# Kernel tuning notes

Measured on AMD Instinct MI355X. Metric: run time of the kernel, lower is better.

The kernel has to match this reference:

```python
import jax, jax.numpy as jnp
import numpy as np

DIM = 1024
T = 16384
WINDOW = 32
DIM_HEAD = 64
HEADS = DIM // DIM_HEAD  # 16
EPS = 1e-5


def setup_inputs() -> dict:
    key = jax.random.key(0)
    k1, k2, k3 = jax.random.split(key, 3)
    x = jax.random.normal(k1, (DIM, T), dtype=jnp.float32)
    w_qkv = jax.random.normal(k2, (3 * DIM, DIM), dtype=jnp.float32) / np.float32(np.sqrt(DIM))
    w_out = jax.random.normal(k3, (DIM, DIM), dtype=jnp.float32) / np.float32(np.sqrt(DIM))
    gamma = jnp.ones((DIM,), dtype=jnp.float32)
    beta = jnp.zeros((DIM,), dtype=jnp.float32)
    return {"x": x, "w_qkv": w_qkv, "w_out": w_out, "gamma": gamma, "beta": beta}


def _rotate_half(t):
    # original: split channels into (2, d/2), swap halves with negation
    d = t.shape[-1]
    return jnp.concatenate((-t[..., d // 2:], t[..., :d // 2]), axis=-1)


def reference(x, w_qkv, w_out, gamma, beta):
    C, Tn = x.shape
    xt = x.T  # (T, C)
    # LayerNorm over channel dim (eqx.nn.LayerNorm, eps=1e-5)
    mu = jnp.mean(xt, axis=-1, keepdims=True)
    var = jnp.var(xt, axis=-1, keepdims=True)
    normed = (xt - mu) * jax.lax.rsqrt(var + EPS) * gamma + beta
    # QKV projection (Linear with weight (out,in), no bias)
    qkv = normed @ w_qkv.T  # (T, 3C)
    q, k, v = jnp.split(qkv, 3, axis=-1)
    w = Tn // WINDOW
    def towin(t):  # (w n) (h d) -> h w n d
        return t.reshape(w, WINDOW, HEADS, DIM_HEAD).transpose(2, 0, 1, 3)
    q, k, v = map(towin, (q, k, v))
    # rotary pos emb over window positions (use_xpos=False -> scale == 1)
    inv_freq = 1.0 / (10000.0 ** (jnp.arange(0, DIM_HEAD, 2, dtype=jnp.float32) / DIM_HEAD))
    tpos = jnp.arange(WINDOW, dtype=jnp.float32)
    freqs = jnp.einsum('i,j->ij', tpos, inv_freq)  # (n, d/2)
    freqs = jnp.concatenate((freqs, freqs), axis=-1)  # (n, d)
    cos, sin = jnp.cos(freqs), jnp.sin(freqs)
    q = q * cos + _rotate_half(q) * sin
    k = k * cos + _rotate_half(k) * sin
    # per-head, per-window full (non-causal) attention
    scale = DIM_HEAD ** -0.5
    logits = jnp.einsum('hwnd,hwmd->hwnm', q, k) * scale
    attn = jax.nn.softmax(logits, axis=-1)
    out = jnp.einsum('hwnm,hwmd->hwnd', attn, v)
    out = out.transpose(1, 2, 0, 3).reshape(Tn, C)  # h w n d -> (w n) (h d)
    out = out @ w_out.T
    return out.T + x
```

## Files before the change

kernel.cpp:

```cpp
#include <hip/hip_runtime.h>

#define T_TOK 16384
#define C_DIM 1024

typedef float f32x4 __attribute__((ext_vector_type(4)));
typedef float f32x16 __attribute__((ext_vector_type(16)));
typedef __bf16 bf16x8 __attribute__((ext_vector_type(8)));
typedef unsigned short u16x8 __attribute__((ext_vector_type(8)));
typedef unsigned short u16x4 __attribute__((ext_vector_type(4)));

__device__ __forceinline__ unsigned short f2bf(float f) {
  union { float f; unsigned u; } v; v.f = f;
  unsigned r = v.u + 0x7fffu + ((v.u >> 16) & 1u);
  return (unsigned short)(r >> 16);
}
__device__ __forceinline__ float bf2f(unsigned short h) {
  union { unsigned u; float f; } v; v.u = ((unsigned)h) << 16;
  return v.f;
}
__device__ __forceinline__ unsigned pk2(float a, float b) {
  return (unsigned)f2bf(a) | ((unsigned)f2bf(b) << 16);
}

__global__ __launch_bounds__(256) void cvt_kernel(const float* __restrict__ in,
                                                  unsigned short* __restrict__ out, int n4) {
  int i = blockIdx.x * 256 + threadIdx.x;
  if (i >= n4) return;
  f32x4 v = *(const f32x4*)(in + (size_t)i * 4);
  u16x4 o;
#pragma unroll
  for (int j = 0; j < 4; ++j) o[j] = f2bf(v[j]);
  *(u16x4*)(out + (size_t)i * 4) = o;
}

__global__ __launch_bounds__(256) void rope_tab_kernel(float* __restrict__ tab) {
  int idx = blockIdx.x * 256 + threadIdx.x;
  if (idx >= 1024) return;
  int mm = idx >> 5, d = idx & 31;
  float invf = powf(10000.f, -(float)d * (1.f / 32.f));
  float ang = (float)mm * invf;
  float s, c;
  sincosf(ang, &s, &c);
  tab[idx * 2] = c;
  tab[idx * 2 + 1] = s;
}

__global__ __launch_bounds__(256) void ln_stats_kernel(const float* __restrict__ x,
                                                       float* __restrict__ mu,
                                                       float* __restrict__ rstd) {
  __shared__ float s1[4][64];
  __shared__ float s2[4][64];
  const int tid = threadIdx.x;
  const int lt = tid & 63, cq = tid >> 6;
  const int t = blockIdx.x * 64 + lt;
  float s = 0.f, ss = 0.f;
  const float* p = x + (size_t)cq * 256 * T_TOK + t;
  for (int c = 0; c < 256; ++c) {
    float v = p[(size_t)c * T_TOK];
    s += v; ss += v * v;
  }
  s1[cq][lt] = s; s2[cq][lt] = ss;
  __syncthreads();
  if (tid < 64) {
    float S  = s1[0][tid] + s1[1][tid] + s1[2][tid] + s1[3][tid];
    float SS = s2[0][tid] + s2[1][tid] + s2[2][tid] + s2[3][tid];
    float m = S * (1.f / 1024.f);
    float var = SS * (1.f / 1024.f) - m * m;
    mu[blockIdx.x * 64 + tid] = m;
    rstd[blockIdx.x * 64 + tid] = rsqrtf(var + 1e-5f);
  }
}

__global__ __launch_bounds__(256) void ln_tr_kernel(const float* __restrict__ x,
                                                    const float* __restrict__ mu,
                                                    const float* __restrict__ rstd,
                                                    const float* __restrict__ gamma,
                                                    const float* __restrict__ beta,
                                                    unsigned short* __restrict__ normed) {
  __shared__ float tile[64][65];
  __shared__ float gs[64], bs[64], ms[64], rs[64];
  const int tid = threadIdx.x;
  const int bt = blockIdx.x & 255;
  const int bc = blockIdx.x >> 8;
  const int t0 = bt * 64, c0 = bc * 64;
  if (tid < 64) {
    gs[tid] = gamma[c0 + tid];
    bs[tid] = beta[c0 + tid];
    ms[tid] = mu[t0 + tid];
    rs[tid] = rstd[t0 + tid];
  }
  const int lc = tid >> 4;
  const int lt4 = (tid & 15) * 4;
#pragma unroll
  for (int r = 0; r < 4; ++r) {
    int c = r * 16 + lc;
    f32x4 v = *(const f32x4*)&x[(size_t)(c0 + c) * T_TOK + t0 + lt4];
    tile[c][lt4 + 0] = v[0]; tile[c][lt4 + 1] = v[1];
    tile[c][lt4 + 2] = v[2]; tile[c][lt4 + 3] = v[3];
  }
  __syncthreads();
#pragma unroll
  for (int r = 0; r < 2; ++r) {
    int idx = r * 256 + tid;
    int t = idx >> 3;
    int c8 = (idx & 7) * 8;
    float m = ms[t], rr = rs[t];
    u16x8 o;
#pragma unroll
    for (int j = 0; j < 8; ++j) {
      float v = tile[c8 + j][t];
      v = (v - m) * rr * gs[c8 + j] + bs[c8 + j];
      o[j] = f2bf(v);
    }
    *(u16x8*)&normed[(size_t)(t0 + t) * C_DIM + c0 + c8] = o;
  }
}

#define GLDS(gp, lp) \
  __builtin_amdgcn_global_load_lds((const __attribute__((address_space(1))) void*)(gp), \
                                   (__attribute__((address_space(3))) void*)(lp), 16, 0, 0)

#define BARF() do { __builtin_amdgcn_s_barrier(); asm volatile("" ::: "memory"); } while (0)
#define VMC(n) asm volatile("s_waitcnt vmcnt(" #n ")" ::: "memory")

__global__ __launch_bounds__(512, 2) void qkvattn_kernel(const unsigned short* __restrict__ A,
                                                         const unsigned short* __restrict__ Bq,
                                                         const float* __restrict__ ropeT,
                                                         unsigned short* __restrict__ aout) {
  __shared__ unsigned short arena[57344];
  unsigned short* LA = arena;
  unsigned short* LB = arena + 32768;
  unsigned short* QKl = arena;
  unsigned short* Vtl = arena + 34816;

  const int tid = threadIdx.x;
  const int w = tid >> 6, lane = tid & 63;
  const int wm = w >> 1, wn = w & 1;
  const int K = 1024, KT = 16;

  const int xcd = blockIdx.x & 7;
  const int ib = blockIdx.x >> 3;
  const int tt = xcd * 8 + (ib & 7);
  const int h = ib >> 3;
  const size_t m0 = (size_t)tt * 256;

  const int preslot = ((lane & 7) ^ (lane >> 3)) * 8;
  const unsigned short* gA = A + (m0 + w * 8 + (lane >> 3)) * (size_t)K + preslot;
  const unsigned short* gB0 = Bq + ((size_t)(0 + h * 64 + w * 8 + (lane >> 3))) * K + preslot;
  const unsigned short* gB1 = Bq + ((size_t)(1024 + h * 64 + w * 8 + (lane >> 3))) * K + preslot;
  const unsigned short* gB2 = Bq + ((size_t)(2048 + h * 64 + w * 8 + (lane >> 3))) * K + preslot;

  auto stage7 = [&](int b, int kt) {
    const size_t k0 = (size_t)kt * 64;
    GLDS(gA + k0,                      LA + b * 16384 + (w * 8) * 64);
    GLDS(gA + (size_t)64 * K + k0,     LA + b * 16384 + (64 + w * 8) * 64);
    GLDS(gA + (size_t)128 * K + k0,    LA + b * 16384 + (128 + w * 8) * 64);
    GLDS(gA + (size_t)192 * K + k0,    LA + b * 16384 + (192 + w * 8) * 64);
    GLDS(gB0 + k0,                     LB + b * 12288 + (w * 8) * 64);
    GLDS(gB1 + k0,                     LB + b * 12288 + (64 + w * 8) * 64);
    GLDS(gB2 + k0,                     LB + b * 12288 + (128 + w * 8) * 64);
  };

  f32x4 acc[4][6];
#pragma unroll
  for (int i = 0; i < 4; ++i)
#pragma unroll
    for (int j = 0; j < 6; ++j) acc[i][j] = (f32x4){0.f, 0.f, 0.f, 0.f};

  const int off_r = (lane & 15) * 64;
  const int slot0 = (((lane >> 4) ^ (lane & 7)) * 8);
  const int slot1 = slot0 ^ 32;

  stage7(0, 0);
  stage7(1, 1);
  VMC(7);
  BARF();

  int bb = 0;
  for (int t = 0; t < KT; ++t, bb ^= 1) {
    const unsigned short* Ab = LA + bb * 16384 + (wm * 64) * 64;
    const unsigned short* Bb = LB + bb * 12288 + (wn * 96) * 64;

    bf16x8 aF[4][2], bF[6][2];
#pragma unroll
    for (int mi = 0; mi < 4; ++mi) {
      aF[mi][0] = *(const bf16x8*)&Ab[mi * 1024 + off_r + slot0];
      aF[mi][1] = *(const bf16x8*)&Ab[mi * 1024 + off_r + slot1];
    }
#pragma unroll
    for (int ni = 0; ni < 6; ++ni) {
      bF[ni][0] = *(const bf16x8*)&Bb[ni * 1024 + off_r + slot0];
      bF[ni][1] = *(const bf16x8*)&Bb[ni * 1024 + off_r + slot1];
    }

    __builtin_amdgcn_s_setprio(1);
#pragma unroll
    for (int mi = 0; mi < 4; ++mi)
#pragma unroll
      for (int ni = 0; ni < 6; ++ni)
#pragma unroll
        for (int ks = 0; ks < 2; ++ks)
          acc[mi][ni] = __builtin_amdgcn_mfma_f32_16x16x32_bf16(aF[mi][ks], bF[ni][ks], acc[mi][ni], 0, 0, 0);
    __builtin_amdgcn_s_setprio(0);
    BARF();

    if (t + 2 < KT) {
      stage7(bb, t + 2);
      VMC(7);
    } else {
      VMC(0);
    }
    BARF();
  }

  __syncthreads();
#pragma unroll
  for (int mi = 0; mi < 4; ++mi)
#pragma unroll
    for (int ni = 0; ni < 6; ++ni) {
      const int j = wn * 96 + ni * 16 + (lane & 15);
#pragma unroll
      for (int r = 0; r < 4; ++r) {
        int tok = wm * 64 + mi * 16 + (lane >> 4) * 4 + r;
        unsigned short bv = f2bf(acc[mi][ni][r]);
        if (wn == 0 || ni < 2) {
          QKl[tok * 136 + j] = bv;
        } else {
          int d = j - 128;
          int mm = tok & 31, win = tok >> 5;
          Vtl[(win * 64 + d) * 32 + ((((mm >> 3) ^ (d ^ (d >> 2))) & 3) * 8 + (mm & 7))] = bv;
        }
      }
    }
  __syncthreads();

  {
    const int m = lane & 31, hi = lane >> 5;
    const unsigned short* qp = QKl + (size_t)(w * 32 + m) * 136;
    u16x8 qv[4], kv[4];
#pragma unroll
    for (int s = 0; s < 4; ++s) {
      int off = s * 16 + hi * 8;
      qv[s] = *(const u16x8*)(qp + off);
      kv[s] = *(const u16x8*)(qp + 64 + off);
    }

    f32x4 ct[2][4];
    const float* tp = ropeT + (size_t)(m * 32 + hi * 8) * 2;
#pragma unroll
    for (int kp = 0; kp < 2; ++kp)
#pragma unroll
      for (int q = 0; q < 4; ++q)
        ct[kp][q] = *(const f32x4*)(tp + kp * 32 + q * 4);

    union FU { unsigned u[4]; bf16x8 v; };
    bf16x8 qfr[4], kfr[4];
#pragma unroll
    for (int ks = 0; ks < 4; ++ks) {
      const int kp = ks & 1;
      FU fq, fk;
#pragma unroll
      for (int jp = 0; jp < 4; ++jp) {
        float c0 = ct[kp][jp][0], s0 = ct[kp][jp][1];
        float c1 = ct[kp][jp][2], s1 = ct[kp][jp][3];
        float q0 = bf2f(qv[ks][2 * jp]), q1 = bf2f(qv[ks][2 * jp + 1]);
        float k0 = bf2f(kv[ks][2 * jp]), k1 = bf2f(kv[ks][2 * jp + 1]);
        float rq0, rq1, rk0, rk1;
        if (ks < 2) {
          rq0 = -bf2f(qv[ks + 2][2 * jp]); rq1 = -bf2f(qv[ks + 2][2 * jp + 1]);
          rk0 = -bf2f(kv[ks + 2][2 * jp]); rk1 = -bf2f(kv[ks + 2][2 * jp + 1]);
        } else {
          rq0 = bf2f(qv[ks - 2][2 * jp]); rq1 = bf2f(qv[ks - 2][2 * jp + 1]);
          rk0 = bf2f(kv[ks - 2][2 * jp]); rk1 = bf2f(kv[ks - 2][2 * jp + 1]);
        }
        fq.u[jp] = pk2(q0 * c0 + rq0 * s0, q1 * c1 + rq1 * s1);
        fk.u[jp] = pk2(k0 * c0 + rk0 * s0, k1 * c1 + rk1 * s1);
      }
      qfr[ks] = fq.v; kfr[ks] = fk.v;
    }

    f32x16 accS;
#pragma unroll
    for (int i = 0; i < 16; ++i) accS[i] = 0.f;
#pragma unroll
    for (int ks = 0; ks < 4; ++ks)
      accS = __builtin_amdgcn_mfma_f32_32x32x16_bf16(kfr[ks], qfr[ks], accS, 0, 0, 0);

    float p[16];
    float mx = -1e30f;
#pragma unroll
    for (int r = 0; r < 16; ++r) { p[r] = accS[r] * 0.125f; mx = fmaxf(mx, p[r]); }
    mx = fmaxf(mx, __shfl_xor(mx, 32, 64));
    float sum = 0.f;
#pragma unroll
    for (int r = 0; r < 16; ++r) { p[r] = __expf(p[r] - mx); sum += p[r]; }
    sum += __shfl_xor(sum, 32, 64);
    const float inv = 1.f / sum;
#pragma unroll
    for (int r = 0; r < 16; ++r) p[r] *= inv;

    bf16x8 pfr[2];
    {
      FU f0, f1;
      unsigned a0 = hi ? pk2(p[0], p[1]) : pk2(p[4], p[5]);
      unsigned a1 = hi ? pk2(p[2], p[3]) : pk2(p[6], p[7]);
      unsigned b0 = (unsigned)__shfl_xor((int)a0, 32, 64);
      unsigned b1 = (unsigned)__shfl_xor((int)a1, 32, 64);
      if (hi) { f0.u[0] = b0; f0.u[1] = b1; f0.u[2] = pk2(p[4], p[5]); f0.u[3] = pk2(p[6], p[7]); }
      else    { f0.u[0] = pk2(p[0], p[1]); f0.u[1] = pk2(p[2], p[3]); f0.u[2] = b0; f0.u[3] = b1; }
      unsigned a2 = hi ? pk2(p[8], p[9])   : pk2(p[12], p[13]);
      unsigned a3 = hi ? pk2(p[10], p[11]) : pk2(p[14], p[15]);
      unsigned b2 = (unsigned)__shfl_xor((int)a2, 32, 64);
      unsigned b3 = (unsigned)__shfl_xor((int)a3, 32, 64);
      if (hi) { f1.u[0] = b2; f1.u[1] = b3; f1.u[2] = pk2(p[12], p[13]); f1.u[3] = pk2(p[14], p[15]); }
      else    { f1.u[0] = pk2(p[8], p[9]); f1.u[1] = pk2(p[10], p[11]); f1.u[2] = b2; f1.u[3] = b3; }
      pfr[0] = f0.v; pfr[1] = f1.v;
    }

    f32x16 accO[2];
#pragma unroll
    for (int i = 0; i < 16; ++i) { accO[0][i] = 0.f; accO[1][i] = 0.f; }
    const int dl = lane & 31;
#pragma unroll
    for (int dh = 0; dh < 2; ++dh) {
      int d = dh * 32 + dl;
      int sx = (d ^ (d >> 2)) & 3;
#pragma unroll
      for (int ks = 0; ks < 2; ++ks) {
        bf16x8 vf = *(const bf16x8*)&Vtl[(w * 64 + d) * 32 + (((2 * ks + hi) ^ sx) & 3) * 8];
        accO[dh] = __builtin_amdgcn_mfma_f32_32x32x16_bf16(pfr[ks], vf, accO[dh], 0, 0, 0);
      }
    }

    const int W = tt * 8 + w;
#pragma unroll
    for (int r = 0; r < 16; ++r) {
      int n = (r & 3) + 8 * (r >> 2) + 4 * hi;
      size_t o = (size_t)(W * 32 + n) * 1024 + h * 64 + dl;
      aout[o] = f2bf(accO[0][r]);
      aout[o + 32] = f2bf(accO[1][r]);
    }
  }
}

template <int EPI>
__global__ __launch_bounds__(512, 2) void gemm8p_kernel(const unsigned short* __restrict__ A,
                                                        const unsigned short* __restrict__ B,
                                                        unsigned short* __restrict__ Obf,
                                                        int ldo, int nbn, int K,
                                                        const float* __restrict__ Xadd,
                                                        float* __restrict__ Ofp) {
  __shared__ unsigned short Lds[2][2][2][8192];
  const int tid = threadIdx.x;
  const int w = tid >> 6, lane = tid & 63;
  const int wm = w >> 2, wn = w & 3;

  const int nbm = gridDim.x / nbn;
  const int xcd = blockIdx.x & 7;
  const int ib = blockIdx.x >> 3;
  int mt, nt;
  if ((nbm & 7) == 0) {
    const int mtpx = nbm >> 3;
    mt = xcd * mtpx + (ib % mtpx);
    nt = ib / mtpx;
  } else {
    const int ntpx = nbn >> 3;
    nt = xcd * ntpx + (ib % ntpx);
    mt = ib / ntpx;
  }
  const size_t m0 = (size_t)mt * 256, n0 = (size_t)nt * 256;

  const unsigned short* gA = A + (m0 + (lane >> 3)) * (size_t)K + ((lane & 7) ^ (lane >> 3)) * 8;
  const unsigned short* gB = B + (n0 + (lane >> 3)) * (size_t)K + ((lane & 7) ^ (lane >> 3)) * 8;
  const int wrow = w * 8;

  auto stageA = [&](int b, int h, int kt) {
    const unsigned short* g = gA + (size_t)(h * 128) * K + (size_t)kt * 64;
    GLDS(g + (size_t)wrow * K,        &Lds[0][b][h][wrow * 64]);
    GLDS(g + (size_t)(64 + wrow) * K, &Lds[0][b][h][(64 + wrow) * 64]);
  };
  auto stageB = [&](int b, int h, int kt) {
    const unsigned short* g = gB + (size_t)(h * 128) * K + (size_t)kt * 64;
    GLDS(g + (size_t)wrow * K,        &Lds[1][b][h][wrow * 64]);
    GLDS(g + (size_t)(64 + wrow) * K, &Lds[1][b][h][(64 + wrow) * 64]);
  };

  f32x4 acc[8][4];
#pragma unroll
  for (int i = 0; i < 8; ++i)
#pragma unroll
    for (int j = 0; j < 4; ++j) acc[i][j] = (f32x4){0.f, 0.f, 0.f, 0.f};

  const int KT = K >> 6;
  const int off_r = (lane & 15) * 64;
  const int slot0 = (((lane >> 4) ^ (lane & 7)) * 8);
  const int slot1 = slot0 ^ 32;
  const int boff = (wn & 1) * 4096;

  bf16x8 aLo[4][2], aHi[4][2], bLo[2][2], bHi[2][2];

  stageA(0, 0, 0); stageA(0, 1, 0); stageB(0, 0, 0); stageB(0, 1, 0);
  if (KT > 1) {
    stageB(1, 0, 1); stageB(1, 1, 1); stageA(1, 0, 1); stageA(1, 1, 1);
    VMC(8);
  } else {
    VMC(0);
  }
  BARF();

  int bb = 0;
  for (int t = 0; t < KT; ++t, bb ^= 1) {
    const unsigned short* Ab = &Lds[0][bb][wm][0];
    const unsigned short* Bb = &Lds[1][bb][wn >> 1][boff];

#pragma unroll
    for (int mi = 0; mi < 4; ++mi) {
      aLo[mi][0] = *(const bf16x8*)&Ab[mi * 1024 + off_r + slot0];
      aLo[mi][1] = *(const bf16x8*)&Ab[mi * 1024 + off_r + slot1];
    }
#pragma unroll
    for (int ni = 0; ni < 2; ++ni) {
      bLo[ni][0] = *(const bf16x8*)&Bb[ni * 1024 + off_r + slot0];
      bLo[ni][1] = *(const bf16x8*)&Bb[ni * 1024 + off_r + slot1];
      bHi[ni][0] = *(const bf16x8*)&Bb[(ni + 2) * 1024 + off_r + slot0];
      bHi[ni][1] = *(const bf16x8*)&Bb[(ni + 2) * 1024 + off_r + slot1];
    }

    __builtin_amdgcn_s_setprio(1);
#pragma unroll
    for (int mi = 0; mi < 4; ++mi)
#pragma unroll
      for (int ni = 0; ni < 2; ++ni)
#pragma unroll
        for (int ks = 0; ks < 2; ++ks)
          acc[mi][ni] = __builtin_amdgcn_mfma_f32_16x16x32_bf16(aLo[mi][ks], bLo[ni][ks], acc[mi][ni], 0, 0, 0);
    __builtin_amdgcn_s_setprio(0);

#pragma unroll
    for (int mi = 0; mi < 4; ++mi) {
      aHi[mi][0] = *(const bf16x8*)&Ab[(mi + 4) * 1024 + off_r + slot0];
      aHi[mi][1] = *(const bf16x8*)&Ab[(mi + 4) * 1024 + off_r + slot1];
    }

    __builtin_amdgcn_s_setprio(1);
#pragma unroll
    for (int mi = 0; mi < 4; ++mi)
#pragma unroll
      for (int ni = 0; ni < 2; ++ni)
#pragma unroll
        for (int ks = 0; ks < 2; ++ks)
          acc[mi][ni + 2] = __builtin_amdgcn_mfma_f32_16x16x32_bf16(aLo[mi][ks], bHi[ni][ks], acc[mi][ni + 2], 0, 0, 0);
    __builtin_amdgcn_s_setprio(0);
    BARF();

    if (t + 2 < KT) { stageB(bb, 0, t + 2); stageB(bb, 1, t + 2); }

    __builtin_amdgcn_s_setprio(1);
#pragma unroll
    for (int mi = 0; mi < 4; ++mi)
#pragma unroll
      for (int ni = 0; ni < 2; ++ni)
#pragma unroll
        for (int ks = 0; ks < 2; ++ks)
          acc[mi + 4][ni + 2] = __builtin_amdgcn_mfma_f32_16x16x32_bf16(aHi[mi][ks], bHi[ni][ks], acc[mi + 4][ni + 2], 0, 0, 0);
    __builtin_amdgcn_s_setprio(0);
    BARF();

    if (t + 2 < KT) { stageA(bb, 0, t + 2); stageA(bb, 1, t + 2); }

    __builtin_amdgcn_s_setprio(1);
#pragma unroll
    for (int mi = 0; mi < 4; ++mi)
#pragma unroll
      for (int ni = 0; ni < 2; ++ni)
#pragma unroll
        for (int ks = 0; ks < 2; ++ks)
          acc[mi + 4][ni] = __builtin_amdgcn_mfma_f32_16x16x32_bf16(aHi[mi][ks], bLo[ni][ks], acc[mi + 4][ni], 0, 0, 0);
    __builtin_amdgcn_s_setprio(0);

    if (t + 2 < KT) {
      VMC(8);
    } else {
      VMC(0);
    }
    BARF();
  }

  if (EPI == 0) {
    unsigned short* cw = &Lds[0][0][0][0] + (size_t)w * 8192;
#pragma unroll
    for (int mi = 0; mi < 8; ++mi)
#pragma unroll
      for (int ni = 0; ni < 4; ++ni)
#pragma unroll
        for (int r = 0; r < 4; ++r)
          cw[(mi * 16 + (lane >> 4) * 4 + r) * 64 + ni * 16 + (lane & 15)] = f2bf(acc[mi][ni][r]);
    const size_t gr0 = m0 + wm * 128;
    const size_t gc0 = n0 + wn * 64;
#pragma unroll
    for (int it = 0; it < 16; ++it) {
      int idx = it * 64 + lane;
      int rr = idx >> 3, c8 = (idx & 7) * 8;
      *(u16x8*)&Obf[(gr0 + rr) * (size_t)ldo + gc0 + c8] = *(const u16x8*)&cw[rr * 64 + c8];
    }
  } else {
    const size_t mrow0 = m0 + wm * 128 + (lane >> 4) * 4;
    const size_t ncol0 = n0 + wn * 64 + (lane & 15);
#pragma unroll
    for (int mi = 0; mi < 8; ++mi)
#pragma unroll
      for (int ni = 0; ni < 4; ++ni)
#pragma unroll
        for (int r = 0; r < 4; ++r) {
          size_t o = (mrow0 + mi * 16 + r) * T_TOK + ncol0 + ni * 16;
          Ofp[o] = acc[mi][ni][r] + Xadd[o];
        }
  }
}

extern "C" void kernel_launch(void* const* d_in, const int* in_sizes, int n_in,
                              void* d_out, int out_size, void* d_ws, size_t ws_size,
                              hipStream_t stream) {
  const float* x     = (const float*)d_in[0];
  const float* w_qkv = (const float*)d_in[1];
  const float* w_out = (const float*)d_in[2];
  const float* gamma = (const float*)d_in[3];
  const float* beta  = (const float*)d_in[4];

  char* ws = (char*)d_ws;
  unsigned short* wqkv_bf = (unsigned short*)(ws);
  unsigned short* wout_bf = (unsigned short*)(ws + 6291456);
  float* mu    = (float*)(ws + 8388608);
  float* rstd  = (float*)(ws + 8454144);
  float* ropeT = (float*)(ws + 8519680);
  unsigned short* normed = (unsigned short*)(ws + 8527872);
  unsigned short* aout   = (unsigned short*)(ws + 42082304);

  cvt_kernel<<<3072, 256, 0, stream>>>(w_qkv, wqkv_bf, 3072 * 1024 / 4);
  cvt_kernel<<<1024, 256, 0, stream>>>(w_out, wout_bf, 1024 * 1024 / 4);
  rope_tab_kernel<<<4, 256, 0, stream>>>(ropeT);
  ln_stats_kernel<<<256, 256, 0, stream>>>(x, mu, rstd);
  ln_tr_kernel<<<4096, 256, 0, stream>>>(x, mu, rstd, gamma, beta, normed);
  qkvattn_kernel<<<1024, 512, 0, stream>>>(normed, wqkv_bf, ropeT, aout);
  gemm8p_kernel<1><<<256, 512, 0, stream>>>(wout_bf, aout, nullptr, 0, 64, 1024,
                                            x, (float*)d_out);
}
```

Measured before the change: 205.8 us.

## Fuse LayerNorm stats and transpose; interleave QKV GEMM loads with MFMA

Two LayerNorm kernels (a stats pass and a normalize-transpose pass) are merged into one kernel. It stages a 1024x32 token tile in LDS, so x is read from HBM once instead of twice and the mu/rstd buffers are dropped. In the QKV GEMM main loop, the A-fragment LDS reads and the next-stage global-to-LDS loads are split into quarters and placed between MFMA groups, with extra barriers, to overlap memory traffic with compute. The fused LN kernel uses about 132KB of LDS per block and only 512 blocks, which limits occupancy, and its first-pass loads are scalar strided 4-byte reads.

Result: faster. 200.3 us (-2.7%).

```diff
diff --git a/kernel.cpp b/kernel.cpp
--- a/kernel.cpp
+++ b/kernel.cpp
@@ -45,74 +45,54 @@
   tab[idx * 2 + 1] = s;
 }
 
-__global__ __launch_bounds__(256) void ln_stats_kernel(const float* __restrict__ x,
-                                                       float* __restrict__ mu,
-                                                       float* __restrict__ rstd) {
-  __shared__ float s1[4][64];
-  __shared__ float s2[4][64];
+__global__ __launch_bounds__(256) void ln_fused_kernel(const float* __restrict__ x,
+                                                       const float* __restrict__ gamma,
+                                                       const float* __restrict__ beta,
+                                                       unsigned short* __restrict__ normed) {
+  __shared__ float tile[1024][33];
+  __shared__ float s1[8][32], s2[8][32];
+  __shared__ float ms[32], rs[32];
   const int tid = threadIdx.x;
-  const int lt = tid & 63, cq = tid >> 6;
-  const int t = blockIdx.x * 64 + lt;
-  float s = 0.f, ss = 0.f;
-  const float* p = x + (size_t)cq * 256 * T_TOK + t;
-  for (int c = 0; c < 256; ++c) {
-    float v = p[(size_t)c * T_TOK];
-    s += v; ss += v * v;
-  }
-  s1[cq][lt] = s; s2[cq][lt] = ss;
+  const int t0 = blockIdx.x * 32;
+
+  {
+    const int tok = tid & 31, g = tid >> 5;
+    float s = 0.f, ss = 0.f;
+    const float* p = x + (size_t)(g * 128) * T_TOK + t0 + tok;
+#pragma unroll 4
+    for (int i = 0; i < 128; ++i) {
+      float v = p[(size_t)i * T_TOK];
+      tile[g * 128 + i][tok] = v;
+      s += v; ss += v * v;
+    }
+    s1[g][tok] = s; s2[g][tok] = ss;
+  }
   __syncthreads();
-  if (tid < 64) {
-    float S  = s1[0][tid] + s1[1][tid] + s1[2][tid] + s1[3][tid];
-    float SS = s2[0][tid] + s2[1][tid] + s2[2][tid] + s2[3][tid];
+  if (tid < 32) {
+    float S = 0.f, SS = 0.f;
+#pragma unroll
+    for (int g = 0; g < 8; ++g) { S += s1[g][tid]; SS += s2[g][tid]; }
     float m = S * (1.f / 1024.f);
     float var = SS * (1.f / 1024.f) - m * m;
-    mu[blockIdx.x * 64 + tid] = m;
-    rstd[blockIdx.x * 64 + tid] = rsqrtf(var + 1e-5f);
-  }
-}
-
-__global__ __launch_bounds__(256) void ln_tr_kernel(const float* __restrict__ x,
-                                                    const float* __restrict__ mu,
-                                                    const float* __restrict__ rstd,
-                                                    const float* __restrict__ gamma,
-                                                    const float* __restrict__ beta,
-                                                    unsigned short* __restrict__ normed) {
-  __shared__ float tile[64][65];
-  __shared__ float gs[64], bs[64], ms[64], rs[64];
-  const int tid = threadIdx.x;
-  const int bt = blockIdx.x & 255;
-  const int bc = blockIdx.x >> 8;
-  const int t0 = bt * 64, c0 = bc * 64;
-  if (tid < 64) {
-    gs[tid] = gamma[c0 + tid];
-    bs[tid] = beta[c0 + tid];
-    ms[tid] = mu[t0 + tid];
-    rs[tid] = rstd[t0 + tid];
-  }
-  const int lc = tid >> 4;
-  const int lt4 = (tid & 15) * 4;
-#pragma unroll
-  for (int r = 0; r < 4; ++r) {
-    int c = r * 16 + lc;
-    f32x4 v = *(const f32x4*)&x[(size_t)(c0 + c) * T_TOK + t0 + lt4];
-    tile[c][lt4 + 0] = v[0]; tile[c][lt4 + 1] = v[1];
-    tile[c][lt4 + 2] = v[2]; tile[c][lt4 + 3] = v[3];
+    ms[tid] = m;
+    rs[tid] = rsqrtf(var + 1e-5f);
   }
   __syncthreads();
-#pragma unroll
-  for (int r = 0; r < 2; ++r) {
-    int idx = r * 256 + tid;
-    int t = idx >> 3;
-    int c8 = (idx & 7) * 8;
-    float m = ms[t], rr = rs[t];
-    u16x8 o;
-#pragma unroll
-    for (int j = 0; j < 8; ++j) {
-      float v = tile[c8 + j][t];
-      v = (v - m) * rr * gs[c8 + j] + bs[c8 + j];
-      o[j] = f2bf(v);
-    }
-    *(u16x8*)&normed[(size_t)(t0 + t) * C_DIM + c0 + c8] = o;
+
+  {
+    const int tok = tid >> 3, cg = tid & 7;
+    const float m = ms[tok], rr = rs[tok];
+#pragma unroll
+    for (int i = 0; i < 16; ++i) {
+      int ch8 = cg * 8 + i * 64;
+      u16x8 o;
+#pragma unroll
+      for (int j = 0; j < 8; ++j) {
+        float v = tile[ch8 + j][tok];
+        o[j] = f2bf((v - m) * rr * gamma[ch8 + j] + beta[ch8 + j]);
+      }
+      *(u16x8*)&normed[(size_t)(t0 + tok) * C_DIM + ch8] = o;
+    }
   }
 }
 
@@ -150,15 +130,18 @@
   const unsigned short* gB1 = Bq + ((size_t)(1024 + h * 64 + w * 8 + (lane >> 3))) * K + preslot;
   const unsigned short* gB2 = Bq + ((size_t)(2048 + h * 64 + w * 8 + (lane >> 3))) * K + preslot;
 
-  auto stage7 = [&](int b, int kt) {
+  auto stageA4 = [&](int b, int kt) {
     const size_t k0 = (size_t)kt * 64;
-    GLDS(gA + k0,                      LA + b * 16384 + (w * 8) * 64);
-    GLDS(gA + (size_t)64 * K + k0,     LA + b * 16384 + (64 + w * 8) * 64);
-    GLDS(gA + (size_t)128 * K + k0,    LA + b * 16384 + (128 + w * 8) * 64);
-    GLDS(gA + (size_t)192 * K + k0,    LA + b * 16384 + (192 + w * 8) * 64);
-    GLDS(gB0 + k0,                     LB + b * 12288 + (w * 8) * 64);
-    GLDS(gB1 + k0,                     LB + b * 12288 + (64 + w * 8) * 64);
-    GLDS(gB2 + k0,                     LB + b * 12288 + (128 + w * 8) * 64);
+    GLDS(gA + k0,                   LA + b * 16384 + (w * 8) * 64);
+    GLDS(gA + (size_t)64 * K + k0,  LA + b * 16384 + (64 + w * 8) * 64);
+    GLDS(gA + (size_t)128 * K + k0, LA + b * 16384 + (128 + w * 8) * 64);
+    GLDS(gA + (size_t)192 * K + k0, LA + b * 16384 + (192 + w * 8) * 64);
+  };
+  auto stageB3 = [&](int b, int kt) {
+    const size_t k0 = (size_t)kt * 64;
+    GLDS(gB0 + k0, LB + b * 12288 + (w * 8) * 64);
+    GLDS(gB1 + k0, LB + b * 12288 + (64 + w * 8) * 64);
+    GLDS(gB2 + k0, LB + b * 12288 + (128 + w * 8) * 64);
   };
 
   f32x4 acc[4][6];
@@ -171,8 +154,10 @@
   const int slot0 = (((lane >> 4) ^ (lane & 7)) * 8);
   const int slot1 = slot0 ^ 32;
 
-  stage7(0, 0);
-  stage7(1, 1);
+  bf16x8 aF[4][2], bF[6][2];
+
+  stageA4(0, 0); stageB3(0, 0);
+  stageA4(1, 1); stageB3(1, 1);
   VMC(7);
   BARF();
 
@@ -181,9 +166,8 @@
     const unsigned short* Ab = LA + bb * 16384 + (wm * 64) * 64;
     const unsigned short* Bb = LB + bb * 12288 + (wn * 96) * 64;
 
-    bf16x8 aF[4][2], bF[6][2];
-#pragma unroll
-    for (int mi = 0; mi < 4; ++mi) {
+#pragma unroll
+    for (int mi = 0; mi < 2; ++mi) {
       aF[mi][0] = *(const bf16x8*)&Ab[mi * 1024 + off_r + slot0];
       aF[mi][1] = *(const bf16x8*)&Ab[mi * 1024 + off_r + slot1];
     }
@@ -195,17 +179,57 @@
 
     __builtin_amdgcn_s_setprio(1);
 #pragma unroll
-    for (int mi = 0; mi < 4; ++mi)
-#pragma unroll
-      for (int ni = 0; ni < 6; ++ni)
+    for (int mi = 0; mi < 2; ++mi)
+#pragma unroll
+      for (int ni = 0; ni < 3; ++ni)
 #pragma unroll
         for (int ks = 0; ks < 2; ++ks)
           acc[mi][ni] = __builtin_amdgcn_mfma_f32_16x16x32_bf16(aF[mi][ks], bF[ni][ks], acc[mi][ni], 0, 0, 0);
     __builtin_amdgcn_s_setprio(0);
+
+#pragma unroll
+    for (int mi = 2; mi < 4; ++mi) {
+      aF[mi][0] = *(const bf16x8*)&Ab[mi * 1024 + off_r + slot0];
+      aF[mi][1] = *(const bf16x8*)&Ab[mi * 1024 + off_r + slot1];
+    }
+
+    __builtin_amdgcn_s_setprio(1);
+#pragma unroll
+    for (int mi = 0; mi < 2; ++mi)
+#pragma unroll
+      for (int ni = 3; ni < 6; ++ni)
+#pragma unroll
+        for (int ks = 0; ks < 2; ++ks)
+          acc[mi][ni] = __builtin_amdgcn_mfma_f32_16x16x32_bf16(aF[mi][ks], bF[ni][ks], acc[mi][ni], 0, 0, 0);
+    __builtin_amdgcn_s_setprio(0);
     BARF();
 
+    if (t + 2 < KT) stageB3(bb, t + 2);
+
+    __builtin_amdgcn_s_setprio(1);
+#pragma unroll
+    for (int mi = 2; mi < 4; ++mi)
+#pragma unroll
+      for (int ni = 3; ni < 6; ++ni)
+#pragma unroll
+        for (int ks = 0; ks < 2; ++ks)
+          acc[mi][ni] = __builtin_amdgcn_mfma_f32_16x16x32_bf16(aF[mi][ks], bF[ni][ks], acc[mi][ni], 0, 0, 0);
+    __builtin_amdgcn_s_setprio(0);
+    BARF();
+
+    if (t + 2 < KT) stageA4(bb, t + 2);
+
+    __builtin_amdgcn_s_setprio(1);
+#pragma unroll
+    for (int mi = 2; mi < 4; ++mi)
+#pragma unroll
+      for (int ni = 0; ni < 3; ++ni)
+#pragma unroll
+        for (int ks = 0; ks < 2; ++ks)
+          acc[mi][ni] = __builtin_amdgcn_mfma_f32_16x16x32_bf16(aF[mi][ks], bF[ni][ks], acc[mi][ni], 0, 0, 0);
+    __builtin_amdgcn_s_setprio(0);
+
     if (t + 2 < KT) {
-      stage7(bb, t + 2);
       VMC(7);
     } else {
       VMC(0);
@@ -530,8 +554,6 @@
   char* ws = (char*)d_ws;
   unsigned short* wqkv_bf = (unsigned short*)(ws);
   unsigned short* wout_bf = (unsigned short*)(ws + 6291456);
-  float* mu    = (float*)(ws + 8388608);
-  float* rstd  = (float*)(ws + 8454144);
   float* ropeT = (float*)(ws + 8519680);
   unsigned short* normed = (unsigned short*)(ws + 8527872);
   unsigned short* aout   = (unsigned short*)(ws + 42082304);
@@ -539,8 +561,7 @@
   cvt_kernel<<<3072, 256, 0, stream>>>(w_qkv, wqkv_bf, 3072 * 1024 / 4);
   cvt_kernel<<<1024, 256, 0, stream>>>(w_out, wout_bf, 1024 * 1024 / 4);
   rope_tab_kernel<<<4, 256, 0, stream>>>(ropeT);
-  ln_stats_kernel<<<256, 256, 0, stream>>>(x, mu, rstd);
-  ln_tr_kernel<<<4096, 256, 0, stream>>>(x, mu, rstd, gamma, beta, normed);
+  ln_fused_kernel<<<512, 256, 0, stream>>>(x, gamma, beta, normed);
   qkvattn_kernel<<<1024, 512, 0, stream>>>(normed, wqkv_bf, ropeT, aout);
   gemm8p_kernel<1><<<256, 512, 0, stream>>>(wout_bf, aout, nullptr, 0, 64, 1024,
                                             x, (float*)d_out);
```
